# Optimization experiments

Hardware: AMD Instinct MI355X
Metric: run time of the kernel (lower is better)

Reference implementation:

```python
import jax, jax.numpy as jnp
import numpy as np

B, R, L = 1, 256, 384
IN_DIM, PAIR_DIM, N_HEADS = 128, 128, 8
HEAD_DIM = IN_DIM // N_HEADS
FF_MULT = 4


def layer_norm(x, g, b, eps=1e-5):
    mu = jnp.mean(x, axis=-1, keepdims=True)
    var = jnp.mean((x - mu) ** 2, axis=-1, keepdims=True)
    return (x - mu) * jax.lax.rsqrt(var + eps) * g + b


def setup_inputs() -> dict:
    key = jax.random.key(0)
    ks = jax.random.split(key, 12)
    s = 0.02
    return {
        "x": jax.random.normal(ks[0], (B, L, L, PAIR_DIM), jnp.float32),
        "m": jax.random.normal(ks[1], (B, R, L, IN_DIM), jnp.float32),
        "ln1_g": jnp.ones((PAIR_DIM,), jnp.float32),
        "ln1_b": jnp.zeros((PAIR_DIM,), jnp.float32),
        "ln2_g": jnp.ones((IN_DIM,), jnp.float32),
        "ln2_b": jnp.zeros((IN_DIM,), jnp.float32),
        "ln3_g": jnp.ones((IN_DIM,), jnp.float32),
        "ln3_b": jnp.zeros((IN_DIM,), jnp.float32),
        "w1": jax.random.normal(ks[2], (PAIR_DIM, N_HEADS), jnp.float32) * s,
        "b1": jnp.zeros((N_HEADS,), jnp.float32),
        "w2": jax.random.normal(ks[3], (IN_DIM, HEAD_DIM), jnp.float32) * s,
        "b2": jnp.zeros((HEAD_DIM,), jnp.float32),
        "ffw1": jax.random.normal(ks[4], (IN_DIM, IN_DIM * FF_MULT), jnp.float32) * s,
        "ffb1": jnp.zeros((IN_DIM * FF_MULT,), jnp.float32),
        "ffw2": jax.random.normal(ks[5], (IN_DIM * FF_MULT, IN_DIM), jnp.float32) * s,
        "ffb2": jnp.zeros((IN_DIM,), jnp.float32),
    }


def reference(x, m, ln1_g, ln1_b, ln2_g, ln2_b, ln3_g, ln3_b,
              w1, b1, w2, b2, ffw1, ffb1, ffw2, ffb2):
    # symmetrize pair features: [b, i, j, d]
    pair = (x + jnp.swapaxes(x, 1, 2)) * 0.5
    pair = layer_norm(pair, ln1_g, ln1_b)
    # attention logits per head, softmax over j (axis=-2): [b, i, j, h]
    attn = jax.nn.softmax(pair @ w1 + b1, axis=-2)
    # values: [b, r, j, d_head]
    values = layer_norm(m, ln2_g, ln2_b) @ w2 + b2
    # [b,i,j,h] x [b,r,j,d] -> [b,r,i,h,d]
    attn_out = jnp.einsum('bijh,brjd->brihd', attn, values)
    attn_out = attn_out.reshape(*attn_out.shape[:3], -1)  # [b,r,i,h*d]
    out = m + attn_out
    residue = layer_norm(out, ln3_g, ln3_b)
    ff = jax.nn.relu(residue @ ffw1 + ffb1) @ ffw2 + ffb2  # dropout off (eval)
    return out + ff
```

## Files before the change

kernel.cpp:

```cpp
#include <hip/hip_runtime.h>

typedef __attribute__((ext_vector_type(8))) short bf16x8;
typedef __attribute__((ext_vector_type(4))) float f32x4;

constexpr int L  = 384;
constexpr int R  = 256;
constexpr int D  = 128;
constexpr int NH = 8;
constexpr int HD = 16;
constexpr int FF = 512;

#define MFMA16(a, b, c) __builtin_amdgcn_mfma_f32_16x16x32_bf16((a), (b), (c), 0, 0, 0)

__device__ inline unsigned short f2bf(float f) {
    unsigned u = __builtin_bit_cast(unsigned, f);
    u += 0x7fffu + ((u >> 16) & 1u);
    return (unsigned short)(u >> 16);
}

__device__ inline int tri_row(int q) {
    int i = (int)((769.0f - sqrtf((float)(591361 - 8 * q))) * 0.5f);
    while ((i + 1) * (769 - (i + 1)) / 2 <= q) ++i;
    while (i * (769 - i) / 2 > q) --i;
    return i;
}

__global__ void k_prep(const float* __restrict__ w1,
                       const float* __restrict__ w2,
                       const float* __restrict__ ffw1,
                       const float* __restrict__ ffw2,
                       const float* __restrict__ g3,
                       const float* __restrict__ b3,
                       const float* __restrict__ ffb1,
                       unsigned short* __restrict__ w1p,
                       unsigned short* __restrict__ w2p,
                       unsigned short* __restrict__ w1gF,
                       unsigned short* __restrict__ w2tF,
                       float2* __restrict__ c1c2) {
    const int idx = blockIdx.x * 256 + threadIdx.x;
    {
        const int fi = idx >> 9, rem = idx & 511, l = rem >> 3, e = rem & 7;
        const int lr2 = l & 15, lg2 = l >> 4;
        const int n = fi >> 2, ks = fi & 3;
        const int ch = n * 16 + lr2, k = ks * 32 + lg2 * 8 + e;
        w1gF[idx] = f2bf(g3[k] * ffw1[(size_t)k * FF + ch]);
    }
    {
        const int fi = idx >> 9, rem = idx & 511, l = rem >> 3, e = rem & 7;
        const int lr2 = l & 15, lg2 = l >> 4;
        const int n = fi >> 4, Ks = fi & 15;
        const int ch = n * 16 + lr2, k = Ks * 32 + lg2 * 8 + e;
        w2tF[idx] = f2bf(ffw2[(size_t)k * D + ch]);
    }
    if (idx < 16 * D) {
        const int n = idx >> 7, k = idx & 127;
        w1p[idx] = (n < NH) ? f2bf(w1[(size_t)k * NH + n]) : (unsigned short)0;
        w2p[idx] = f2bf(w2[(size_t)k * HD + n]);
    }
    if (blockIdx.x < 2) {
        const int n = blockIdx.x * 256 + threadIdx.x;
        float c1 = 0.f, c2 = 0.f;
        for (int k = 0; k < D; ++k) {
            const float w = ffw1[(size_t)k * FF + n];
            c1 += g3[k] * w;
            c2 += b3[k] * w;
        }
        c1c2[n] = make_float2(c1, c2 + ffb1[n]);
    }
}

__global__ void k_pair_logits(const float* __restrict__ x,
                              const float* __restrict__ g,
                              const float* __restrict__ bt,
                              const unsigned short* __restrict__ w1p,
                              const float* __restrict__ b1,
                              float* __restrict__ logits) {
    __shared__ unsigned short nrm[64][136];
    __shared__ int ij[64];
    const int tid = threadIdx.x;
    const int q0 = blockIdx.x * 64;

    {
        const int pr = tid >> 2, part = tid & 3;
        const int q = q0 + pr;
        const int i = tri_row(q);
        const int j = i + (q - i * (769 - i) / 2);
        if (part == 0) ij[pr] = (i << 16) | j;
        const float* xa = x + ((size_t)i * L + j) * D + part * 32;
        const float* xb = x + ((size_t)j * L + i) * D + part * 32;
        float v[32];
        float s = 0.f, sq = 0.f;
        #pragma unroll
        for (int q8 = 0; q8 < 8; ++q8) {
            const float4 a = ((const float4*)xa)[q8];
            const float4 b = ((const float4*)xb)[q8];
            const float t0 = 0.5f * (a.x + b.x), t1 = 0.5f * (a.y + b.y);
            const float t2 = 0.5f * (a.z + b.z), t3 = 0.5f * (a.w + b.w);
            v[q8*4+0] = t0; v[q8*4+1] = t1; v[q8*4+2] = t2; v[q8*4+3] = t3;
            s  += t0 + t1 + t2 + t3;
            sq += t0*t0 + t1*t1 + t2*t2 + t3*t3;
        }
        s  += __shfl_xor(s, 1);  s  += __shfl_xor(s, 2);
        sq += __shfl_xor(sq, 1); sq += __shfl_xor(sq, 2);
        const float mean = s * (1.0f / D);
        const float rstd = rsqrtf(sq * (1.0f / D) - mean * mean + 1e-5f);
        #pragma unroll
        for (int q8 = 0; q8 < 8; ++q8) {
            const int c = part * 32 + q8 * 4;
            ushort4 pk;
            pk.x = f2bf((v[q8*4+0] - mean) * rstd * g[c+0] + bt[c+0]);
            pk.y = f2bf((v[q8*4+1] - mean) * rstd * g[c+1] + bt[c+1]);
            pk.z = f2bf((v[q8*4+2] - mean) * rstd * g[c+2] + bt[c+2]);
            pk.w = f2bf((v[q8*4+3] - mean) * rstd * g[c+3] + bt[c+3]);
            *(ushort4*)(&nrm[pr][c]) = pk;
        }
    }
    __syncthreads();

    {
        const int wv = tid >> 6, lane = tid & 63;
        const int lr = lane & 15, lg = lane >> 4;
        f32x4 acc = {0.f, 0.f, 0.f, 0.f};
        #pragma unroll
        for (int ks = 0; ks < 4; ++ks) {
            bf16x8 a = *(const bf16x8*)(&nrm[wv * 16 + lr][ks * 32 + lg * 8]);
            bf16x8 b = *(const bf16x8*)(w1p + (size_t)lr * D + ks * 32 + lg * 8);
            acc = MFMA16(a, b, acc);
        }
        if (lr < NH) {
            #pragma unroll
            for (int r = 0; r < 4; ++r) {
                const int pl = wv * 16 + lg * 4 + r;
                const int pij = ij[pl];
                const int pi = pij >> 16, pj = pij & 0xffff;
                const float val = acc[r] + b1[lr];
                logits[((size_t)pi * L + pj) * NH + lr] = val;
                logits[((size_t)pj * L + pi) * NH + lr] = val;
            }
        }
    }
}

__global__ void k_softmax(const float* __restrict__ logits,
                          unsigned short* __restrict__ attnT) {
    const int wave = blockIdx.x * 4 + (threadIdx.x >> 6);
    const int lane = threadIdx.x & 63;
    const int i = wave >> 3, h = wave & 7;

    float v[6];
    float mx = -1e30f;
    #pragma unroll
    for (int t = 0; t < 6; ++t) {
        const int j = lane + t * 64;
        v[t] = logits[((size_t)i * L + j) * NH + h];
        mx = fmaxf(mx, v[t]);
    }
    #pragma unroll
    for (int msk = 32; msk; msk >>= 1) mx = fmaxf(mx, __shfl_xor(mx, msk));

    float s = 0.0f;
    #pragma unroll
    for (int t = 0; t < 6; ++t) { v[t] = __expf(v[t] - mx); s += v[t]; }
    #pragma unroll
    for (int msk = 32; msk; msk >>= 1) s += __shfl_xor(s, msk);
    const float inv = 1.0f / s;

    #pragma unroll
    for (int t = 0; t < 6; ++t) {
        const int j = lane + t * 64;
        attnT[((size_t)h * L + i) * L + j] = f2bf(v[t] * inv);
    }
}

__global__ void k_values(const float* __restrict__ min_,
                         const float* __restrict__ g,
                         const float* __restrict__ bt,
                         const unsigned short* __restrict__ w2p,
                         const float* __restrict__ b2,
                         unsigned short* __restrict__ VtT) {
    __shared__ unsigned short nrm[128][136];
    const int tid = threadIdx.x;
    const int r  = blockIdx.x;
    const int j0 = blockIdx.y * 128;

    #pragma unroll
    for (int half = 0; half < 2; ++half) {
        const int row  = half * 64 + (tid >> 2);
        const int part = tid & 3;
        const float* src = min_ + ((size_t)r * L + j0 + row) * D + part * 32;
        float v[32];
        float s = 0.f, sq = 0.f;
        #pragma unroll
        for (int q = 0; q < 8; ++q) {
            const float4 a = ((const float4*)src)[q];
            v[q*4+0] = a.x; v[q*4+1] = a.y; v[q*4+2] = a.z; v[q*4+3] = a.w;
            s  += a.x + a.y + a.z + a.w;
            sq += a.x*a.x + a.y*a.y + a.z*a.z + a.w*a.w;
        }
        s  += __shfl_xor(s, 1);  s  += __shfl_xor(s, 2);
        sq += __shfl_xor(sq, 1); sq += __shfl_xor(sq, 2);
        const float mean = s * (1.0f / D);
        const float rstd = rsqrtf(sq * (1.0f / D) - mean * mean + 1e-5f);
        #pragma unroll
        for (int q = 0; q < 8; ++q) {
            const int c = part * 32 + q * 4;
            ushort4 pk;
            pk.x = f2bf((v[q*4+0] - mean) * rstd * g[c+0] + bt[c+0]);
            pk.y = f2bf((v[q*4+1] - mean) * rstd * g[c+1] + bt[c+1]);
            pk.z = f2bf((v[q*4+2] - mean) * rstd * g[c+2] + bt[c+2]);
            pk.w = f2bf((v[q*4+3] - mean) * rstd * g[c+3] + bt[c+3]);
            *(ushort4*)(&nrm[row][c]) = pk;
        }
    }
    __syncthreads();

    {
        const int wv = tid >> 6, lane = tid & 63;
        const int lr = lane & 15, lg = lane >> 4;
        f32x4 acc[2];
        acc[0] = (f32x4){0.f, 0.f, 0.f, 0.f};
        acc[1] = (f32x4){0.f, 0.f, 0.f, 0.f};
        #pragma unroll
        for (int ks = 0; ks < 4; ++ks) {
            bf16x8 b = *(const bf16x8*)(w2p + (size_t)lr * D + ks * 32 + lg * 8);
            #pragma unroll
            for (int mt = 0; mt < 2; ++mt) {
                bf16x8 a = *(const bf16x8*)(&nrm[wv * 32 + mt * 16 + lr][ks * 32 + lg * 8]);
                acc[mt] = MFMA16(a, b, acc[mt]);
            }
        }
        const float bb = b2[lr];
        #pragma unroll
        for (int mt = 0; mt < 2; ++mt) {
            ushort4 pk;
            pk.x = f2bf(acc[mt][0] + bb);
            pk.y = f2bf(acc[mt][1] + bb);
            pk.z = f2bf(acc[mt][2] + bb);
            pk.w = f2bf(acc[mt][3] + bb);
            *(ushort4*)(VtT + (size_t)(r * HD + lr) * L + j0 + wv * 32 + mt * 16 + lg * 4) = pk;
        }
    }
}

__global__ void k_attn_out(const unsigned short* __restrict__ attnT,
                           const unsigned short* __restrict__ VtT,
                           const float* __restrict__ min_,
                           float* __restrict__ out) {
    const int h  = blockIdx.z;
    const int i0 = blockIdx.x * 128;
    const int n0 = blockIdx.y * 128;
    const int tid = threadIdx.x, wv = tid >> 6, lane = tid & 63;
    const int lr = lane & 15, lg = lane >> 4;
    const int wio = (wv >> 1) * 64, wno = (wv & 1) * 64;
    const unsigned short* Abase = attnT + (size_t)h * L * L;

    f32x4 acc[4][4];
    #pragma unroll
    for (int a = 0; a < 4; ++a)
        #pragma unroll
        for (int b = 0; b < 4; ++b) acc[a][b] = (f32x4){0.f, 0.f, 0.f, 0.f};

    bf16x8 af[4], bf[4], afn[4], bfn[4];
    #pragma unroll
    for (int mt = 0; mt < 4; ++mt)
        af[mt] = *(const bf16x8*)(Abase + (size_t)(i0 + wio + mt * 16 + lr) * L + lg * 8);
    #pragma unroll
    for (int nt = 0; nt < 4; ++nt)
        bf[nt] = *(const bf16x8*)(VtT + (size_t)(n0 + wno + nt * 16 + lr) * L + lg * 8);

    for (int ks = 0; ks < 12; ++ks) {
        if (ks < 11) {
            const int ko = (ks + 1) * 32 + lg * 8;
            #pragma unroll
            for (int mt = 0; mt < 4; ++mt)
                afn[mt] = *(const bf16x8*)(Abase + (size_t)(i0 + wio + mt * 16 + lr) * L + ko);
            #pragma unroll
            for (int nt = 0; nt < 4; ++nt)
                bfn[nt] = *(const bf16x8*)(VtT + (size_t)(n0 + wno + nt * 16 + lr) * L + ko);
        }
        #pragma unroll
        for (int mt = 0; mt < 4; ++mt)
            #pragma unroll
            for (int nt = 0; nt < 4; ++nt)
                acc[mt][nt] = MFMA16(af[mt], bf[nt], acc[mt][nt]);
        #pragma unroll
        for (int q = 0; q < 4; ++q) { af[q] = afn[q]; bf[q] = bfn[q]; }
    }

    #pragma unroll
    for (int mt = 0; mt < 4; ++mt) {
        #pragma unroll
        for (int nt = 0; nt < 4; ++nt) {
            const int nbase = n0 + wno + nt * 16;
            const int rrow  = nbase >> 4;
            #pragma unroll
            for (int r = 0; r < 4; ++r) {
                const int i = i0 + wio + mt * 16 + lg * 4 + r;
                const size_t gidx = ((size_t)rrow * L + i) * D + h * HD + lr;
                out[gidx] = min_[gidx] + acc[mt][nt][r];
            }
        }
    }
}

__global__ __launch_bounds__(512, 4) void k_ffn(
                      const unsigned short* __restrict__ w1gF,
                      const float2* __restrict__ c1c2,
                      const unsigned short* __restrict__ w2tF,
                      const float* __restrict__ ffb2,
                      float* out) {
    __shared__ unsigned short At[64 * 128];
    __shared__ unsigned short hid[2][64 * 128];
    __shared__ float2 stats[64];
    const int tid = threadIdx.x;
    const size_t row0 = (size_t)blockIdx.x * 64;

    const int wv = tid >> 6, lane = tid & 63;
    const int lr = lane & 15, lg = lane >> 4;
    const int wm = wv >> 2, wn = wv & 3;

    bf16x8 w1f[8], w2f[8];
    #pragma unroll
    for (int ks = 0; ks < 4; ++ks)
        #pragma unroll
        for (int nt = 0; nt < 2; ++nt) {
            const int fi = (0 * 8 + wn * 2 + nt) * 4 + ks;
            w1f[ks * 2 + nt] = *(const bf16x8*)((const char*)w1gF + fi * 1024 + lane * 16);
        }

    {
        const int rr = tid >> 3, part = tid & 7;
        const float* src = out + (row0 + rr) * D + part * 16;
        const float4 a0 = ((const float4*)src)[0];
        const float4 a1 = ((const float4*)src)[1];
        const float4 a2 = ((const float4*)src)[2];
        const float4 a3 = ((const float4*)src)[3];
        float s  = a0.x+a0.y+a0.z+a0.w + a1.x+a1.y+a1.z+a1.w
                 + a2.x+a2.y+a2.z+a2.w + a3.x+a3.y+a3.z+a3.w;
        float sq = a0.x*a0.x+a0.y*a0.y+a0.z*a0.z+a0.w*a0.w
                 + a1.x*a1.x+a1.y*a1.y+a1.z*a1.z+a1.w*a1.w
                 + a2.x*a2.x+a2.y*a2.y+a2.z*a2.z+a2.w*a2.w
                 + a3.x*a3.x+a3.y*a3.y+a3.z*a3.z+a3.w*a3.w;
        s  += __shfl_xor(s, 1);  s  += __shfl_xor(s, 2);  s  += __shfl_xor(s, 4);
        sq += __shfl_xor(sq, 1); sq += __shfl_xor(sq, 2); sq += __shfl_xor(sq, 4);
        if (part == 0) {
            const float mean = s * (1.0f / D);
            const float rstd = rsqrtf(sq * (1.0f / D) - mean * mean + 1e-5f);
            stats[rr] = make_float2(rstd, mean * rstd);
        }
        const int xr = (rr & 7) << 4;
        char* rowp = (char*)(At + rr * 128);
        ushort4 p0, p1, p2, p3;
        p0.x = f2bf(a0.x); p0.y = f2bf(a0.y); p0.z = f2bf(a0.z); p0.w = f2bf(a0.w);
        p1.x = f2bf(a1.x); p1.y = f2bf(a1.y); p1.z = f2bf(a1.z); p1.w = f2bf(a1.w);
        p2.x = f2bf(a2.x); p2.y = f2bf(a2.y); p2.z = f2bf(a2.z); p2.w = f2bf(a2.w);
        p3.x = f2bf(a3.x); p3.y = f2bf(a3.y); p3.z = f2bf(a3.z); p3.w = f2bf(a3.w);
        const int cb = part * 32;
        *(ushort4*)(rowp + ((cb     ) ^ xr)) = p0;
        *(ushort4*)(rowp + ((cb +  8) ^ xr)) = p1;
        *(ushort4*)(rowp + ((cb + 16) ^ xr)) = p2;
        *(ushort4*)(rowp + ((cb + 24) ^ xr)) = p3;
    }

    #pragma unroll
    for (int ks = 0; ks < 4; ++ks)
        #pragma unroll
        for (int nt = 0; nt < 2; ++nt) {
            const int fi = (wn * 2 + nt) * 16 + 0 * 4 + ks;
            w2f[ks * 2 + nt] = *(const bf16x8*)((const char*)w2tF + fi * 1024 + lane * 16);
        }

    __syncthreads();

    f32x4 acc2[2][2];
    #pragma unroll
    for (int m = 0; m < 2; ++m)
        #pragma unroll
        for (int n = 0; n < 2; ++n) acc2[m][n] = (f32x4){0.f, 0.f, 0.f, 0.f};

    #pragma unroll
    for (int kc = 0; kc < 4; ++kc) {
        const int p = kc & 1;

        {
            f32x4 acc1[2][2];
            #pragma unroll
            for (int m = 0; m < 2; ++m)
                #pragma unroll
                for (int n = 0; n < 2; ++n) acc1[m][n] = (f32x4){0.f, 0.f, 0.f, 0.f};

            #pragma unroll
            for (int ks = 0; ks < 4; ++ks) {
                bf16x8 af[2];
                #pragma unroll
                for (int mt = 0; mt < 2; ++mt) {
                    const int row = wm * 32 + mt * 16 + lr;
                    af[mt] = *(const bf16x8*)((char*)(At + row * 128) +
                              ((ks * 64 + lg * 16) ^ ((row & 7) << 4)));
                }
                #pragma unroll
                for (int mt = 0; mt < 2; ++mt)
                    #pragma unroll
                    for (int nt = 0; nt < 2; ++nt)
                        acc1[mt][nt] = MFMA16(af[mt], w1f[ks * 2 + nt], acc1[mt][nt]);
            }

            #pragma unroll
            for (int nt = 0; nt < 2; ++nt) {
                const int chl = wn * 32 + nt * 16 + lr;
                const float2 cc = c1c2[kc * 128 + chl];
                #pragma unroll
                for (int mt = 0; mt < 2; ++mt) {
                    #pragma unroll
                    for (int r = 0; r < 4; ++r) {
                        const int row = wm * 32 + mt * 16 + lg * 4 + r;
                        const float2 st = stats[row];
                        const float pre = st.x * acc1[mt][nt][r] - st.y * cc.x + cc.y;
                        *(unsigned short*)((char*)(hid[p] + row * 128) +
                            ((chl * 2) ^ ((row & 7) << 4))) = f2bf(fmaxf(pre, 0.f));
                    }
                }
            }
        }
        __syncthreads();

        if (kc < 3) {
            #pragma unroll
            for (int ks = 0; ks < 4; ++ks)
                #pragma unroll
                for (int nt = 0; nt < 2; ++nt) {
                    const int fi = ((kc + 1) * 8 + wn * 2 + nt) * 4 + ks;
                    w1f[ks * 2 + nt] = *(const bf16x8*)((const char*)w1gF + fi * 1024 + lane * 16);
                }
        }

        {
            #pragma unroll
            for (int ks = 0; ks < 4; ++ks) {
                bf16x8 hf[2];
                #pragma unroll
                for (int mt = 0; mt < 2; ++mt) {
                    const int row = wm * 32 + mt * 16 + lr;
                    hf[mt] = *(const bf16x8*)((char*)(hid[p] + row * 128) +
                              ((ks * 64 + lg * 16) ^ ((row & 7) << 4)));
                }
                #pragma unroll
                for (int mt = 0; mt < 2; ++mt)
                    #pragma unroll
                    for (int nt = 0; nt < 2; ++nt)
                        acc2[mt][nt] = MFMA16(hf[mt], w2f[ks * 2 + nt], acc2[mt][nt]);
            }
        }

        if (kc < 3) {
            #pragma unroll
            for (int ks = 0; ks < 4; ++ks)
                #pragma unroll
                for (int nt = 0; nt < 2; ++nt) {
                    const int fi = (wn * 2 + nt) * 16 + (kc + 1) * 4 + ks;
                    w2f[ks * 2 + nt] = *(const bf16x8*)((const char*)w2tF + fi * 1024 + lane * 16);
                }
        }
    }

    #pragma unroll
    for (int nt = 0; nt < 2; ++nt) {
        const int ch = wn * 32 + nt * 16 + lr;
        const float bb = ffb2[ch];
        #pragma unroll
        for (int mt = 0; mt < 2; ++mt) {
            #pragma unroll
            for (int r = 0; r < 4; ++r) {
                const size_t gi = (row0 + wm * 32 + mt * 16 + lg * 4 + r) * (size_t)D + ch;
                out[gi] = out[gi] + acc2[mt][nt][r] + bb;
            }
        }
    }
}

extern "C" void kernel_launch(void* const* d_in, const int* in_sizes, int n_in,
                              void* d_out, int out_size, void* d_ws, size_t ws_size,
                              hipStream_t stream) {
    const float* x     = (const float*)d_in[0];
    const float* m     = (const float*)d_in[1];
    const float* ln1_g = (const float*)d_in[2];
    const float* ln1_b = (const float*)d_in[3];
    const float* ln2_g = (const float*)d_in[4];
    const float* ln2_b = (const float*)d_in[5];
    const float* ln3_g = (const float*)d_in[6];
    const float* ln3_b = (const float*)d_in[7];
    const float* w1    = (const float*)d_in[8];
    const float* b1    = (const float*)d_in[9];
    const float* w2    = (const float*)d_in[10];
    const float* b2    = (const float*)d_in[11];
    const float* ffw1  = (const float*)d_in[12];
    const float* ffb1  = (const float*)d_in[13];
    const float* ffw2  = (const float*)d_in[14];
    const float* ffb2  = (const float*)d_in[15];

    float* out = (float*)d_out;

    char* wsp = (char*)d_ws;
    float*          logits = (float*)wsp;              wsp += (size_t)L*L*NH*4;
    unsigned short* attnT  = (unsigned short*)wsp;     wsp += (size_t)NH*L*L*2;
    unsigned short* VtT    = (unsigned short*)wsp;     wsp += (size_t)R*HD*L*2;
    unsigned short* w1gF   = (unsigned short*)wsp;     wsp += (size_t)FF*D*2;
    unsigned short* w2tF   = (unsigned short*)wsp;     wsp += (size_t)D*FF*2;
    unsigned short* w1p    = (unsigned short*)wsp;     wsp += (size_t)16*D*2;
    unsigned short* w2p    = (unsigned short*)wsp;     wsp += (size_t)16*D*2;
    float2*         c1c2   = (float2*)wsp;             wsp += (size_t)FF*8;

    k_prep<<<(FF * D) / 256, 256, 0, stream>>>(w1, w2, ffw1, ffw2,
                                               ln3_g, ln3_b, ffb1,
                                               w1p, w2p, w1gF, w2tF, c1c2);

    k_pair_logits<<<1155, 256, 0, stream>>>(x, ln1_g, ln1_b, w1p, b1, logits);
    k_softmax<<<(L * NH) / 4, 256, 0, stream>>>(logits, attnT);

    dim3 g3(R, L / 128);
    k_values<<<g3, 256, 0, stream>>>(m, ln2_g, ln2_b, w2p, b2, VtT);

    dim3 g4(L / 128, (R * HD) / 128, NH);
    k_attn_out<<<g4, 256, 0, stream>>>(attnT, VtT, m, out);

    k_ffn<<<(R * L) / 64, 512, 0, stream>>>(w1gF, c1c2, w2tF, ffb2, out);
}
```

Before: 152.7 us.

## Halve FFN row tile to 32 rows and swizzle attention-output block order

```diff
diff --git a/kernel.cpp b/kernel.cpp
--- a/kernel.cpp
+++ b/kernel.cpp
@@ -246,9 +246,13 @@
                            const unsigned short* __restrict__ VtT,
                            const float* __restrict__ min_,
                            float* __restrict__ out) {
-    const int h  = blockIdx.z;
-    const int i0 = blockIdx.x * 128;
-    const int n0 = blockIdx.y * 128;
+    const int orig = blockIdx.x;
+    const int swz  = (orig & 7) * 96 + (orig >> 3);
+    const int h    = swz / 96;
+    const int rem  = swz % 96;
+    const int n0   = (rem / 3) * 128;
+    const int i0   = (rem % 3) * 128;
+
     const int tid = threadIdx.x, wv = tid >> 6, lane = tid & 63;
     const int lr = lane & 15, lg = lane >> 4;
     const int wio = (wv >> 1) * 64, wno = (wv & 1) * 64;
@@ -303,17 +307,17 @@
     }
 }
 
-__global__ __launch_bounds__(512, 4) void k_ffn(
+__global__ __launch_bounds__(512, 8) void k_ffn(
                       const unsigned short* __restrict__ w1gF,
                       const float2* __restrict__ c1c2,
                       const unsigned short* __restrict__ w2tF,
                       const float* __restrict__ ffb2,
                       float* out) {
-    __shared__ unsigned short At[64 * 128];
-    __shared__ unsigned short hid[2][64 * 128];
-    __shared__ float2 stats[64];
+    __shared__ unsigned short At[32 * 128];
+    __shared__ unsigned short hid[2][32 * 128];
+    __shared__ float2 stats[32];
     const int tid = threadIdx.x;
-    const size_t row0 = (size_t)blockIdx.x * 64;
+    const size_t row0 = (size_t)blockIdx.x * 32;
 
     const int wv = tid >> 6, lane = tid & 63;
     const int lr = lane & 15, lg = lane >> 4;
@@ -329,20 +333,17 @@
         }
 
     {
-        const int rr = tid >> 3, part = tid & 7;
-        const float* src = out + (row0 + rr) * D + part * 16;
+        const int rr = tid >> 4, part = tid & 15;
+        const float* src = out + (row0 + rr) * D + part * 8;
         const float4 a0 = ((const float4*)src)[0];
         const float4 a1 = ((const float4*)src)[1];
-        const float4 a2 = ((const float4*)src)[2];
-        const float4 a3 = ((const float4*)src)[3];
-        float s  = a0.x+a0.y+a0.z+a0.w + a1.x+a1.y+a1.z+a1.w
-                 + a2.x+a2.y+a2.z+a2.w + a3.x+a3.y+a3.z+a3.w;
+        float s  = a0.x+a0.y+a0.z+a0.w + a1.x+a1.y+a1.z+a1.w;
         float sq = a0.x*a0.x+a0.y*a0.y+a0.z*a0.z+a0.w*a0.w
-                 + a1.x*a1.x+a1.y*a1.y+a1.z*a1.z+a1.w*a1.w
-                 + a2.x*a2.x+a2.y*a2.y+a2.z*a2.z+a2.w*a2.w
-                 + a3.x*a3.x+a3.y*a3.y+a3.z*a3.z+a3.w*a3.w;
-        s  += __shfl_xor(s, 1);  s  += __shfl_xor(s, 2);  s  += __shfl_xor(s, 4);
-        sq += __shfl_xor(sq, 1); sq += __shfl_xor(sq, 2); sq += __shfl_xor(sq, 4);
+                 + a1.x*a1.x+a1.y*a1.y+a1.z*a1.z+a1.w*a1.w;
+        s  += __shfl_xor(s, 1);  s  += __shfl_xor(s, 2);
+        s  += __shfl_xor(s, 4);  s  += __shfl_xor(s, 8);
+        sq += __shfl_xor(sq, 1); sq += __shfl_xor(sq, 2);
+        sq += __shfl_xor(sq, 4); sq += __shfl_xor(sq, 8);
         if (part == 0) {
             const float mean = s * (1.0f / D);
             const float rstd = rsqrtf(sq * (1.0f / D) - mean * mean + 1e-5f);
@@ -350,16 +351,12 @@
         }
         const int xr = (rr & 7) << 4;
         char* rowp = (char*)(At + rr * 128);
-        ushort4 p0, p1, p2, p3;
-        p0.x = f2bf(a0.x); p0.y = f2bf(a0.y); p0.z = f2bf(a0.z); p0.w = f2bf(a0.w);
-        p1.x = f2bf(a1.x); p1.y = f2bf(a1.y); p1.z = f2bf(a1.z); p1.w = f2bf(a1.w);
-        p2.x = f2bf(a2.x); p2.y = f2bf(a2.y); p2.z = f2bf(a2.z); p2.w = f2bf(a2.w);
-        p3.x = f2bf(a3.x); p3.y = f2bf(a3.y); p3.z = f2bf(a3.z); p3.w = f2bf(a3.w);
-        const int cb = part * 32;
-        *(ushort4*)(rowp + ((cb     ) ^ xr)) = p0;
-        *(ushort4*)(rowp + ((cb +  8) ^ xr)) = p1;
-        *(ushort4*)(rowp + ((cb + 16) ^ xr)) = p2;
-        *(ushort4*)(rowp + ((cb + 24) ^ xr)) = p3;
+        unsigned q0 = (unsigned)f2bf(a0.x) | ((unsigned)f2bf(a0.y) << 16);
+        unsigned q1 = (unsigned)f2bf(a0.z) | ((unsigned)f2bf(a0.w) << 16);
+        unsigned q2 = (unsigned)f2bf(a1.x) | ((unsigned)f2bf(a1.y) << 16);
+        unsigned q3 = (unsigned)f2bf(a1.z) | ((unsigned)f2bf(a1.w) << 16);
+        uint4 pk = {q0, q1, q2, q3};
+        *(uint4*)(rowp + ((part * 16) ^ xr)) = pk;
     }
 
     #pragma unroll
@@ -372,37 +369,26 @@
 
     __syncthreads();
 
-    f32x4 acc2[2][2];
-    #pragma unroll
-    for (int m = 0; m < 2; ++m)
-        #pragma unroll
-        for (int n = 0; n < 2; ++n) acc2[m][n] = (f32x4){0.f, 0.f, 0.f, 0.f};
+    f32x4 acc2[2];
+    acc2[0] = (f32x4){0.f, 0.f, 0.f, 0.f};
+    acc2[1] = (f32x4){0.f, 0.f, 0.f, 0.f};
 
     #pragma unroll
     for (int kc = 0; kc < 4; ++kc) {
         const int p = kc & 1;
 
         {
-            f32x4 acc1[2][2];
-            #pragma unroll
-            for (int m = 0; m < 2; ++m)
-                #pragma unroll
-                for (int n = 0; n < 2; ++n) acc1[m][n] = (f32x4){0.f, 0.f, 0.f, 0.f};
+            f32x4 acc1[2];
+            acc1[0] = (f32x4){0.f, 0.f, 0.f, 0.f};
+            acc1[1] = (f32x4){0.f, 0.f, 0.f, 0.f};
 
             #pragma unroll
             for (int ks = 0; ks < 4; ++ks) {
-                bf16x8 af[2];
-                #pragma unroll
-                for (int mt = 0; mt < 2; ++mt) {
-                    const int row = wm * 32 + mt * 16 + lr;
-                    af[mt] = *(const bf16x8*)((char*)(At + row * 128) +
-                              ((ks * 64 + lg * 16) ^ ((row & 7) << 4)));
-                }
-                #pragma unroll
-                for (int mt = 0; mt < 2; ++mt)
-                    #pragma unroll
-                    for (int nt = 0; nt < 2; ++nt)
-                        acc1[mt][nt] = MFMA16(af[mt], w1f[ks * 2 + nt], acc1[mt][nt]);
+                const int row = wm * 16 + lr;
+                bf16x8 af = *(const bf16x8*)((char*)(At + row * 128) +
+                             ((ks * 64 + lg * 16) ^ ((row & 7) << 4)));
+                acc1[0] = MFMA16(af, w1f[ks * 2 + 0], acc1[0]);
+                acc1[1] = MFMA16(af, w1f[ks * 2 + 1], acc1[1]);
             }
 
             #pragma unroll
@@ -410,15 +396,12 @@
                 const int chl = wn * 32 + nt * 16 + lr;
                 const float2 cc = c1c2[kc * 128 + chl];
                 #pragma unroll
-                for (int mt = 0; mt < 2; ++mt) {
-                    #pragma unroll
-                    for (int r = 0; r < 4; ++r) {
-                        const int row = wm * 32 + mt * 16 + lg * 4 + r;
-                        const float2 st = stats[row];
-                        const float pre = st.x * acc1[mt][nt][r] - st.y * cc.x + cc.y;
-                        *(unsigned short*)((char*)(hid[p] + row * 128) +
-                            ((chl * 2) ^ ((row & 7) << 4))) = f2bf(fmaxf(pre, 0.f));
-                    }
+                for (int r = 0; r < 4; ++r) {
+                    const int row = wm * 16 + lg * 4 + r;
+                    const float2 st = stats[row];
+                    const float pre = st.x * acc1[nt][r] - st.y * cc.x + cc.y;
+                    *(unsigned short*)((char*)(hid[p] + row * 128) +
+                        ((chl * 2) ^ ((row & 7) << 4))) = f2bf(fmaxf(pre, 0.f));
                 }
             }
         }
@@ -437,18 +420,11 @@
         {
             #pragma unroll
             for (int ks = 0; ks < 4; ++ks) {
-                bf16x8 hf[2];
-                #pragma unroll
-                for (int mt = 0; mt < 2; ++mt) {
-                    const int row = wm * 32 + mt * 16 + lr;
-                    hf[mt] = *(const bf16x8*)((char*)(hid[p] + row * 128) +
-                              ((ks * 64 + lg * 16) ^ ((row & 7) << 4)));
-                }
-                #pragma unroll
-                for (int mt = 0; mt < 2; ++mt)
-                    #pragma unroll
-                    for (int nt = 0; nt < 2; ++nt)
-                        acc2[mt][nt] = MFMA16(hf[mt], w2f[ks * 2 + nt], acc2[mt][nt]);
+                const int row = wm * 16 + lr;
+                bf16x8 hf = *(const bf16x8*)((char*)(hid[p] + row * 128) +
+                             ((ks * 64 + lg * 16) ^ ((row & 7) << 4)));
+                acc2[0] = MFMA16(hf, w2f[ks * 2 + 0], acc2[0]);
+                acc2[1] = MFMA16(hf, w2f[ks * 2 + 1], acc2[1]);
             }
         }
 
@@ -468,12 +444,9 @@
         const int ch = wn * 32 + nt * 16 + lr;
         const float bb = ffb2[ch];
         #pragma unroll
-        for (int mt = 0; mt < 2; ++mt) {
-            #pragma unroll
-            for (int r = 0; r < 4; ++r) {
-                const size_t gi = (row0 + wm * 32 + mt * 16 + lg * 4 + r) * (size_t)D + ch;
-                out[gi] = out[gi] + acc2[mt][nt][r] + bb;
-            }
+        for (int r = 0; r < 4; ++r) {
+            const size_t gi = (row0 + wm * 16 + lg * 4 + r) * (size_t)D + ch;
+            out[gi] = out[gi] + acc2[nt][r] + bb;
         }
     }
 }
@@ -520,8 +493,7 @@
     dim3 g3(R, L / 128);
     k_values<<<g3, 256, 0, stream>>>(m, ln2_g, ln2_b, w2p, b2, VtT);
 
-    dim3 g4(L / 128, (R * HD) / 128, NH);
-    k_attn_out<<<g4, 256, 0, stream>>>(attnT, VtT, m, out);
-
-    k_ffn<<<(R * L) / 64, 512, 0, stream>>>(w1gF, c1c2, w2tF, ffb2, out);
-}
+    k_attn_out<<<768, 256, 0, stream>>>(attnT, VtT, m, out);
+
+    k_ffn<<<(R * L) / 32, 512, 0, stream>>>(w1gF, c1c2, w2tF, ffb2, out);
+}
```

After: 314.2 us. 2.06x slower.
